# Kernel optimization log

Hardware: AMD Instinct MI355X
Metric: run time of the kernel (lower is better)

Reference implementation:

```python
import jax, jax.numpy as jnp
import numpy as np

NEG_SLOPE = 0.2
F_OUT = 64


def setup_inputs() -> dict:
    key = jax.random.key(0)
    k1, k2, k3 = jax.random.split(key, 3)
    N, F_IN = 8192, 256
    h = jax.random.normal(k1, (N, F_IN), dtype=jnp.float32)
    adj = jnp.ones((N, N), dtype=jnp.bool_)  # unused by the original forward
    # xavier-uniform-ish init scale
    W = jax.random.uniform(k2, (F_IN, F_OUT), dtype=jnp.float32,
                           minval=-1.0, maxval=1.0) * np.sqrt(6.0 / (F_IN + F_OUT))
    a = jax.random.uniform(k3, (2 * F_OUT, 1), dtype=jnp.float32,
                           minval=-1.0, maxval=1.0) * np.sqrt(6.0 / (2 * F_OUT + 1))
    return {"h": h, "adj": adj, "W": W, "a": a}


def reference(h, adj, W, a):
    # Wh: [N, F_OUT]
    Wh = h @ W
    # The torch code materializes an [N*N, F] repeat to compute what is just
    # a broadcast add of two projected score vectors:
    # e[i, j] = leakyrelu(Wh[i] @ a1 + Wh[j] @ a2)
    s1 = Wh @ a[:F_OUT]   # [N, 1]
    s2 = Wh @ a[F_OUT:]   # [N, 1]
    e = s1 + s2.T         # [N, N]
    e = jnp.where(e >= 0, e, NEG_SLOPE * e)  # LeakyReLU(0.2)
    attention = jax.nn.softmax(e, axis=1)    # note: adj is NOT used (matches source)
    return attention @ Wh                    # [N, F_OUT]
```

## Files before the change

### kernel.cpp

```cpp
#include <hip/hip_runtime.h>
#include <math.h>

#define GN 8192
#define GF 64
#define GFIN 256
#define NEG 0.2f
#define NFINE 256
#define FCH 32

#define OFF_WH   0
#define OFF_S1   (GN*GF)
#define OFF_S2   (OFF_S1 + GN)
#define OFF_ZS   (OFF_S2 + GN)
#define OFF_IDX  (OFF_ZS + GN)
#define OFF_FA   (OFF_IDX + GN)
#define OFF_FB   (OFF_FA + NFINE*GF)
#define OFF_FSA  (OFF_FB + NFINE*GF)
#define OFF_FSB  (OFF_FSA + NFINE)
#define OFF_OFA  (OFF_FSB + NFINE)
#define OFF_OFB  (OFF_OFA + NFINE*GF)
#define OFF_OSA  (OFF_OFB + NFINE*GF)
#define OFF_OSB  (OFF_OSA + NFINE)
#define ZERO_CNT (2*NFINE*GF + 2*NFINE)

__global__ __launch_bounds__(512) void k_wh(const float* __restrict__ h,
        const float* __restrict__ W, const float* __restrict__ a,
        float* __restrict__ wsf) {
    float* Wh = wsf + OFF_WH;
    float* s1 = wsf + OFF_S1;
    float* s2 = wsf + OFF_S2;
    __shared__ float WlT[GF*GFIN];
    int t = threadIdx.x, b = blockIdx.x;
    int zm = b*512 + t;
    if (zm < ZERO_CNT) wsf[OFF_FA + zm] = 0.f;
    int lane = t & 63;
    const float4* W4 = (const float4*)W;
    #pragma unroll
    for (int m = 0; m < 8; ++m) {
        int g = t + m*512;
        float4 v = W4[g];
        int k = g >> 4;
        int c0 = (g & 15) * 4;
        WlT[(c0  )*GFIN + (k ^ (((c0  )&7)<<2))] = v.x;
        WlT[(c0+1)*GFIN + (k ^ (((c0+1)&7)<<2))] = v.y;
        WlT[(c0+2)*GFIN + (k ^ (((c0+2)&7)<<2))] = v.z;
        WlT[(c0+3)*GFIN + (k ^ (((c0+3)&7)<<2))] = v.w;
    }
    __syncthreads();
    int wid = __builtin_amdgcn_readfirstlane(t >> 6);
    int row0 = b*32 + wid*4;
    const float* hrow = h + (size_t)row0 * GFIN;
    float acc[4] = {0.f,0.f,0.f,0.f};
    const float4* WlT4 = (const float4*)WlT;
    int cbase = lane * (GFIN/4);
    int sw = lane & 7;
    #pragma unroll 8
    for (int k4 = 0; k4 < GFIN/4; ++k4) {
        float4 wv = WlT4[cbase + (k4 ^ sw)];
        int kk = k4*4;
        #pragma unroll
        for (int q = 0; q < 4; ++q) {
            acc[q] += hrow[q*GFIN + kk  ] * wv.x;
            acc[q] += hrow[q*GFIN + kk+1] * wv.y;
            acc[q] += hrow[q*GFIN + kk+2] * wv.z;
            acc[q] += hrow[q*GFIN + kk+3] * wv.w;
        }
    }
    float a1 = a[lane], a2 = a[GF + lane];
    #pragma unroll
    for (int q = 0; q < 4; ++q) {
        int row = row0 + q;
        Wh[(size_t)row*GF + lane] = acc[q];
        float v1 = acc[q]*a1, v2 = acc[q]*a2;
        #pragma unroll
        for (int o = 32; o > 0; o >>= 1) { v1 += __shfl_xor(v1, o); v2 += __shfl_xor(v2, o); }
        if (lane == 0) { s1[row] = v1; s2[row] = v2; }
    }
}

__global__ __launch_bounds__(512) void k_rank(const float* __restrict__ Whg,
        float* __restrict__ wsf) {
    __shared__ float zl[GN];
    __shared__ int rl[32];
    __shared__ float redm[8];
    const float* s2 = wsf + OFF_S2;
    float* zs = wsf + OFF_ZS;
    int* idx = (int*)(wsf + OFF_IDX);
    float* fineA = wsf + OFF_FA;
    float* fineB = wsf + OFF_FB;
    float* fSA = wsf + OFF_FSA;
    float* fSB = wsf + OFF_FSB;
    int t = threadIdx.x, b = blockIdx.x;
    int lane = t & 63, wid = t >> 6;
    const float4* s4 = (const float4*)s2;
    float4* z4 = (float4*)zl;
    float mx = -1e30f;
    for (int m = t; m < GN/4; m += 512) {
        float4 v = s4[m]; z4[m] = v;
        mx = fmaxf(fmaxf(mx, v.x), fmaxf(fmaxf(v.y, v.z), v.w));
    }
    #pragma unroll
    for (int o = 32; o > 0; o >>= 1) mx = fmaxf(mx, __shfl_xor(mx, o));
    if (lane == 0) redm[wid] = mx;
    __syncthreads();
    float Z = redm[0];
    #pragma unroll
    for (int w2 = 1; w2 < 8; ++w2) Z = fmaxf(Z, redm[w2]);
    int jl = t >> 4, sl = t & 15;
    int j = b*32 + jl;
    float zj = zl[j];
    int cnt = 0;
    #pragma unroll 4
    for (int i = 0; i < GN/64; ++i) {
        int m4 = i*16 + sl;
        float4 v = z4[m4];
        int mb = m4*4;
        cnt += (v.x < zj) || (v.x == zj && mb   < j);
        cnt += (v.y < zj) || (v.y == zj && mb+1 < j);
        cnt += (v.z < zj) || (v.z == zj && mb+2 < j);
        cnt += (v.w < zj) || (v.w == zj && mb+3 < j);
    }
    cnt += __shfl_xor(cnt, 1);
    cnt += __shfl_xor(cnt, 2);
    cnt += __shfl_xor(cnt, 4);
    cnt += __shfl_xor(cnt, 8);
    if (sl == 0) { zs[cnt] = zj; idx[cnt] = j; rl[jl] = cnt; }
    __syncthreads();
    #pragma unroll
    for (int q = 0; q < 4; ++q) {
        int jj = wid*4 + q;
        int jg = b*32 + jj;
        int r = rl[jj];
        float d = zl[jg] - Z;
        float tA = __expf(d);
        float tB = __expf(NEG*d);
        float w = Whg[(size_t)jg*GF + lane];
        int fc = r >> 5;
        atomicAdd(&fineA[fc*GF + lane], tA*w);
        atomicAdd(&fineB[fc*GF + lane], tB*w);
        if (lane == 0) atomicAdd(&fSA[fc], tA);
        if (lane == 1) atomicAdd(&fSB[fc], tB);
    }
}

__global__ __launch_bounds__(256) void k_scan(float* __restrict__ wsf) {
    __shared__ float stg[NFINE];
    __shared__ float wred[4];
    const float* fineA = wsf + OFF_FA;
    const float* fineB = wsf + OFF_FB;
    const float* fSA = wsf + OFF_FSA;
    const float* fSB = wsf + OFF_FSB;
    float* ofA = wsf + OFF_OFA;
    float* ofB = wsf + OFF_OFB;
    float* osA = wsf + OFF_OSA;
    float* osB = wsf + OFF_OSB;
    int c = blockIdx.x;
    int t = threadIdx.x, lane = t & 63, wid = t >> 6;
    float fA = (c < 64) ? fineA[t*GF + c] : fSA[t];
    float fB = (c < 64) ? fineB[t*GF + c] : fSB[t];
    {
        float ws = fB;
        #pragma unroll
        for (int o = 1; o < 64; o <<= 1) { float y = __shfl_up(ws, o); if (lane >= o) ws += y; }
        if (lane == 63) wred[wid] = ws;
        __syncthreads();
        float blkoff = 0.f;
        #pragma unroll
        for (int w2 = 0; w2 < 4; ++w2) { float x = wred[w2]; if (w2 < wid) blkoff += x; }
        float exB = blkoff + ws - fB;
        if (c < 64) ofB[t*GF + c] = exB; else osB[t] = exB;
    }
    __syncthreads();
    stg[t] = fA;
    __syncthreads();
    {
        int rt = NFINE-1-t;
        float vA = stg[rt];
        float ws = vA;
        #pragma unroll
        for (int o = 1; o < 64; o <<= 1) { float y = __shfl_up(ws, o); if (lane >= o) ws += y; }
        __syncthreads();
        if (lane == 63) wred[wid] = ws;
        __syncthreads();
        float blkoff = 0.f;
        #pragma unroll
        for (int w2 = 0; w2 < 4; ++w2) { float x = wred[w2]; if (w2 < wid) blkoff += x; }
        float exA = blkoff + ws - vA;
        if (c < 64) ofA[rt*GF + c] = exA; else osA[rt] = exA;
    }
}

__global__ __launch_bounds__(256) void k_out(const float* __restrict__ wsf,
        float* __restrict__ out) {
    const float* Wh = wsf + OFF_WH;
    const float* s1 = wsf + OFF_S1;
    const float* zs = wsf + OFF_ZS;
    const int* idx = (const int*)(wsf + OFF_IDX);
    const float* ofA = wsf + OFF_OFA;
    const float* ofB = wsf + OFF_OFB;
    const float* osA = wsf + OFF_OSA;
    const float* osB = wsf + OFF_OSB;
    int t = threadIdx.x;
    int wid = t >> 6, lane = t & 63;
    int i = blockIdx.x*4 + wid;
    float s1i = s1[i];
    float Z = zs[GN-1];
    float g = s1i + Z;
    float m = (g >= 0.f) ? g : NEG*g;
    float aA = __expf(g - m);
    float aB = __expf(NEG*g - m);
    float tgt = -s1i;
    int lo = 0, hi = GN;
    #pragma unroll
    for (int it = 0; it < 13; ++it) {
        int mid = (lo + hi) >> 1;
        if (zs[mid] < tgt) lo = mid + 1; else hi = mid;
    }
    int k = lo;
    int fc = __builtin_amdgcn_readfirstlane(min(k >> 5, NFINE-1));
    float va = ofA[fc*GF + lane];
    float vb = ofB[fc*GF + lane];
    float sa = osA[fc], pb = osB[fc];
    #pragma unroll 8
    for (int q = 0; q < FCH; ++q) {
        int r = fc*FCH + q;
        float zr = zs[r];
        int ir = idx[r];
        float w = Wh[(size_t)ir*GF + lane];
        float d = zr - Z;
        if (r >= k) { float tA = __expf(d);     va += tA*w; sa += tA; }
        else        { float tB = __expf(NEG*d); vb += tB*w; pb += tB; }
    }
    out[(size_t)i*GF + lane] = (aA*va + aB*vb) / (aA*sa + aB*pb);
}

extern "C" void kernel_launch(void* const* d_in, const int* in_sizes, int n_in,
                              void* d_out, int out_size, void* d_ws, size_t ws_size,
                              hipStream_t stream) {
    const float* h = (const float*)d_in[0];
    const float* W = (const float*)d_in[2];
    const float* a = (const float*)d_in[3];
    float* wsf = (float*)d_ws;
    float* out = (float*)d_out;

    hipLaunchKernelGGL(k_wh,   dim3(GN/32), dim3(512), 0, stream, h, W, a, wsf);
    hipLaunchKernelGGL(k_rank, dim3(GN/32), dim3(512), 0, stream, wsf + OFF_WH, wsf);
    hipLaunchKernelGGL(k_scan, dim3(65),    dim3(256), 0, stream, wsf);
    hipLaunchKernelGGL(k_out,  dim3(GN/4),  dim3(256), 0, stream, wsf, out);
}
```

Measured before the change: 70.99 us.

## Fuse scan into rank kernel via last-block pattern and simplify Wh matmul

Removes the separate k_scan launch. The last k_rank block to finish, detected with an atomic counter, now computes the prefix and suffix scans over the fine chunk sums. Separately, k_wh drops the swizzled transposed LDS layout for W, uses 256 threads per block, and computes 8 rows per wave with broadcast LDS reads. The aim is to save one launch and its gap and to cheapen the W staging. In exchange the scan runs serially in a single block at the tail of k_rank.

Measured after the change: 181.7 us. +156.0%, slower.

```diff
diff --git a/kernel.cpp b/kernel.cpp
--- a/kernel.cpp
+++ b/kernel.cpp
@@ -7,6 +7,7 @@
 #define NEG 0.2f
 #define NFINE 256
 #define FCH 32
+#define NBLK_RANK 256
 
 #define OFF_WH   0
 #define OFF_S1   (GN*GF)
@@ -17,58 +18,42 @@
 #define OFF_FB   (OFF_FA + NFINE*GF)
 #define OFF_FSA  (OFF_FB + NFINE*GF)
 #define OFF_FSB  (OFF_FSA + NFINE)
-#define OFF_OFA  (OFF_FSB + NFINE)
+#define OFF_CNT  (OFF_FSB + NFINE)
+#define OFF_OFA  (OFF_CNT + 1)
 #define OFF_OFB  (OFF_OFA + NFINE*GF)
 #define OFF_OSA  (OFF_OFB + NFINE*GF)
 #define OFF_OSB  (OFF_OSA + NFINE)
-#define ZERO_CNT (2*NFINE*GF + 2*NFINE)
-
-__global__ __launch_bounds__(512) void k_wh(const float* __restrict__ h,
+#define ZERO_CNT (2*NFINE*GF + 2*NFINE + 1)
+
+__global__ __launch_bounds__(256) void k_wh(const float* __restrict__ h,
         const float* __restrict__ W, const float* __restrict__ a,
         float* __restrict__ wsf) {
     float* Wh = wsf + OFF_WH;
     float* s1 = wsf + OFF_S1;
     float* s2 = wsf + OFF_S2;
-    __shared__ float WlT[GF*GFIN];
+    __shared__ float Wl[GFIN*GF];
     int t = threadIdx.x, b = blockIdx.x;
-    int zm = b*512 + t;
+    int lane = t & 63;
+    int zm = b*256 + t;
     if (zm < ZERO_CNT) wsf[OFF_FA + zm] = 0.f;
-    int lane = t & 63;
     const float4* W4 = (const float4*)W;
-    #pragma unroll
-    for (int m = 0; m < 8; ++m) {
-        int g = t + m*512;
-        float4 v = W4[g];
-        int k = g >> 4;
-        int c0 = (g & 15) * 4;
-        WlT[(c0  )*GFIN + (k ^ (((c0  )&7)<<2))] = v.x;
-        WlT[(c0+1)*GFIN + (k ^ (((c0+1)&7)<<2))] = v.y;
-        WlT[(c0+2)*GFIN + (k ^ (((c0+2)&7)<<2))] = v.z;
-        WlT[(c0+3)*GFIN + (k ^ (((c0+3)&7)<<2))] = v.w;
-    }
+    float4* Wl4 = (float4*)Wl;
+    #pragma unroll
+    for (int m = 0; m < 16; ++m) Wl4[t + m*256] = W4[t + m*256];
     __syncthreads();
     int wid = __builtin_amdgcn_readfirstlane(t >> 6);
-    int row0 = b*32 + wid*4;
+    int row0 = b*32 + wid*8;
     const float* hrow = h + (size_t)row0 * GFIN;
-    float acc[4] = {0.f,0.f,0.f,0.f};
-    const float4* WlT4 = (const float4*)WlT;
-    int cbase = lane * (GFIN/4);
-    int sw = lane & 7;
+    float acc[8] = {0.f,0.f,0.f,0.f,0.f,0.f,0.f,0.f};
     #pragma unroll 8
-    for (int k4 = 0; k4 < GFIN/4; ++k4) {
-        float4 wv = WlT4[cbase + (k4 ^ sw)];
-        int kk = k4*4;
-        #pragma unroll
-        for (int q = 0; q < 4; ++q) {
-            acc[q] += hrow[q*GFIN + kk  ] * wv.x;
-            acc[q] += hrow[q*GFIN + kk+1] * wv.y;
-            acc[q] += hrow[q*GFIN + kk+2] * wv.z;
-            acc[q] += hrow[q*GFIN + kk+3] * wv.w;
-        }
+    for (int k = 0; k < GFIN; ++k) {
+        float wv = Wl[k*GF + lane];
+        #pragma unroll
+        for (int q = 0; q < 8; ++q) acc[q] += hrow[q*GFIN + k] * wv;
     }
     float a1 = a[lane], a2 = a[GF + lane];
     #pragma unroll
-    for (int q = 0; q < 4; ++q) {
+    for (int q = 0; q < 8; ++q) {
         int row = row0 + q;
         Wh[(size_t)row*GF + lane] = acc[q];
         float v1 = acc[q]*a1, v2 = acc[q]*a2;
@@ -83,6 +68,7 @@
     __shared__ float zl[GN];
     __shared__ int rl[32];
     __shared__ float redm[8];
+    __shared__ int lastBlk;
     const float* s2 = wsf + OFF_S2;
     float* zs = wsf + OFF_ZS;
     int* idx = (int*)(wsf + OFF_IDX);
@@ -90,6 +76,11 @@
     float* fineB = wsf + OFF_FB;
     float* fSA = wsf + OFF_FSA;
     float* fSB = wsf + OFF_FSB;
+    int* cnt = (int*)(wsf + OFF_CNT);
+    float* ofA = wsf + OFF_OFA;
+    float* ofB = wsf + OFF_OFB;
+    float* osA = wsf + OFF_OSA;
+    float* osB = wsf + OFF_OSB;
     int t = threadIdx.x, b = blockIdx.x;
     int lane = t & 63, wid = t >> 6;
     const float4* s4 = (const float4*)s2;
@@ -109,22 +100,22 @@
     int jl = t >> 4, sl = t & 15;
     int j = b*32 + jl;
     float zj = zl[j];
-    int cnt = 0;
+    int c0 = 0;
     #pragma unroll 4
     for (int i = 0; i < GN/64; ++i) {
         int m4 = i*16 + sl;
         float4 v = z4[m4];
         int mb = m4*4;
-        cnt += (v.x < zj) || (v.x == zj && mb   < j);
-        cnt += (v.y < zj) || (v.y == zj && mb+1 < j);
-        cnt += (v.z < zj) || (v.z == zj && mb+2 < j);
-        cnt += (v.w < zj) || (v.w == zj && mb+3 < j);
-    }
-    cnt += __shfl_xor(cnt, 1);
-    cnt += __shfl_xor(cnt, 2);
-    cnt += __shfl_xor(cnt, 4);
-    cnt += __shfl_xor(cnt, 8);
-    if (sl == 0) { zs[cnt] = zj; idx[cnt] = j; rl[jl] = cnt; }
+        c0 += (v.x < zj) || (v.x == zj && mb   < j);
+        c0 += (v.y < zj) || (v.y == zj && mb+1 < j);
+        c0 += (v.z < zj) || (v.z == zj && mb+2 < j);
+        c0 += (v.w < zj) || (v.w == zj && mb+3 < j);
+    }
+    c0 += __shfl_xor(c0, 1);
+    c0 += __shfl_xor(c0, 2);
+    c0 += __shfl_xor(c0, 4);
+    c0 += __shfl_xor(c0, 8);
+    if (sl == 0) { zs[c0] = zj; idx[c0] = j; rl[jl] = c0; }
     __syncthreads();
     #pragma unroll
     for (int q = 0; q < 4; ++q) {
@@ -141,52 +132,46 @@
         if (lane == 0) atomicAdd(&fSA[fc], tA);
         if (lane == 1) atomicAdd(&fSB[fc], tB);
     }
-}
-
-__global__ __launch_bounds__(256) void k_scan(float* __restrict__ wsf) {
-    __shared__ float stg[NFINE];
-    __shared__ float wred[4];
-    const float* fineA = wsf + OFF_FA;
-    const float* fineB = wsf + OFF_FB;
-    const float* fSA = wsf + OFF_FSA;
-    const float* fSB = wsf + OFF_FSB;
-    float* ofA = wsf + OFF_OFA;
-    float* ofB = wsf + OFF_OFB;
-    float* osA = wsf + OFF_OSA;
-    float* osB = wsf + OFF_OSB;
-    int c = blockIdx.x;
-    int t = threadIdx.x, lane = t & 63, wid = t >> 6;
-    float fA = (c < 64) ? fineA[t*GF + c] : fSA[t];
-    float fB = (c < 64) ? fineB[t*GF + c] : fSB[t];
-    {
-        float ws = fB;
+    __threadfence();
+    __syncthreads();
+    if (t == 0) lastBlk = (atomicAdd(cnt, 1) == NBLK_RANK-1);
+    __syncthreads();
+    if (!lastBlk) return;
+    for (int c = wid; c <= 64; c += 8) {
+        float v[4];
+        int p0 = lane*4;
+        #pragma unroll
+        for (int e = 0; e < 4; ++e) {
+            int ch = p0 + e;
+            v[e] = atomicAdd((c < 64) ? &fineB[ch*GF + c] : &fSB[ch], 0.f);
+        }
+        float s = v[0]+v[1]+v[2]+v[3];
+        float ws = s;
         #pragma unroll
         for (int o = 1; o < 64; o <<= 1) { float y = __shfl_up(ws, o); if (lane >= o) ws += y; }
-        if (lane == 63) wred[wid] = ws;
-        __syncthreads();
-        float blkoff = 0.f;
-        #pragma unroll
-        for (int w2 = 0; w2 < 4; ++w2) { float x = wred[w2]; if (w2 < wid) blkoff += x; }
-        float exB = blkoff + ws - fB;
-        if (c < 64) ofB[t*GF + c] = exB; else osB[t] = exB;
-    }
-    __syncthreads();
-    stg[t] = fA;
-    __syncthreads();
-    {
-        int rt = NFINE-1-t;
-        float vA = stg[rt];
-        float ws = vA;
+        float run = ws - s;
+        #pragma unroll
+        for (int e = 0; e < 4; ++e) {
+            int ch = p0 + e;
+            if (c < 64) ofB[ch*GF + c] = run; else osB[ch] = run;
+            run += v[e];
+        }
+        #pragma unroll
+        for (int e = 0; e < 4; ++e) {
+            int ch = NFINE-1 - (p0 + e);
+            v[e] = atomicAdd((c < 64) ? &fineA[ch*GF + c] : &fSA[ch], 0.f);
+        }
+        s = v[0]+v[1]+v[2]+v[3];
+        ws = s;
         #pragma unroll
         for (int o = 1; o < 64; o <<= 1) { float y = __shfl_up(ws, o); if (lane >= o) ws += y; }
-        __syncthreads();
-        if (lane == 63) wred[wid] = ws;
-        __syncthreads();
-        float blkoff = 0.f;
-        #pragma unroll
-        for (int w2 = 0; w2 < 4; ++w2) { float x = wred[w2]; if (w2 < wid) blkoff += x; }
-        float exA = blkoff + ws - vA;
-        if (c < 64) ofA[rt*GF + c] = exA; else osA[rt] = exA;
+        run = ws - s;
+        #pragma unroll
+        for (int e = 0; e < 4; ++e) {
+            int ch = NFINE-1 - (p0 + e);
+            if (c < 64) ofA[ch*GF + c] = run; else osA[ch] = run;
+            run += v[e];
+        }
     }
 }
 
@@ -243,8 +228,7 @@
     float* wsf = (float*)d_ws;
     float* out = (float*)d_out;
 
-    hipLaunchKernelGGL(k_wh,   dim3(GN/32), dim3(512), 0, stream, h, W, a, wsf);
+    hipLaunchKernelGGL(k_wh,   dim3(GN/32), dim3(256), 0, stream, h, W, a, wsf);
     hipLaunchKernelGGL(k_rank, dim3(GN/32), dim3(512), 0, stream, wsf + OFF_WH, wsf);
-    hipLaunchKernelGGL(k_scan, dim3(65),    dim3(256), 0, stream, wsf);
     hipLaunchKernelGGL(k_out,  dim3(GN/4),  dim3(256), 0, stream, wsf, out);
 }
```

## Restructure Wh projection: 8 rows per wave, untransposed W in LDS

Applied to the files above, without the earlier changes.

The projection kernel now uses 256-thread blocks with 4 waves, and each wave computes 8 rows instead of 4. W is copied into shared memory as-is, without the swizzled transpose, and each lane reads one W element per k. This removes the transpose-store overhead and doubles per-wave reuse of each W load across rows. The cost is more accumulators, scalar rather than float4 LDS reads, and fewer threads per block.

Result: slower. 72.62 us (+2.3%).

```diff
diff --git a/kernel.cpp b/kernel.cpp
--- a/kernel.cpp
+++ b/kernel.cpp
@@ -23,52 +23,35 @@
 #define OFF_OSB  (OFF_OSA + NFINE)
 #define ZERO_CNT (2*NFINE*GF + 2*NFINE)
 
-__global__ __launch_bounds__(512) void k_wh(const float* __restrict__ h,
+__global__ __launch_bounds__(256) void k_wh(const float* __restrict__ h,
         const float* __restrict__ W, const float* __restrict__ a,
         float* __restrict__ wsf) {
     float* Wh = wsf + OFF_WH;
     float* s1 = wsf + OFF_S1;
     float* s2 = wsf + OFF_S2;
-    __shared__ float WlT[GF*GFIN];
+    __shared__ float Wl[GFIN*GF];
     int t = threadIdx.x, b = blockIdx.x;
-    int zm = b*512 + t;
+    int lane = t & 63;
+    int zm = b*256 + t;
     if (zm < ZERO_CNT) wsf[OFF_FA + zm] = 0.f;
-    int lane = t & 63;
     const float4* W4 = (const float4*)W;
-    #pragma unroll
-    for (int m = 0; m < 8; ++m) {
-        int g = t + m*512;
-        float4 v = W4[g];
-        int k = g >> 4;
-        int c0 = (g & 15) * 4;
-        WlT[(c0  )*GFIN + (k ^ (((c0  )&7)<<2))] = v.x;
-        WlT[(c0+1)*GFIN + (k ^ (((c0+1)&7)<<2))] = v.y;
-        WlT[(c0+2)*GFIN + (k ^ (((c0+2)&7)<<2))] = v.z;
-        WlT[(c0+3)*GFIN + (k ^ (((c0+3)&7)<<2))] = v.w;
-    }
+    float4* Wl4 = (float4*)Wl;
+    #pragma unroll
+    for (int m = 0; m < 16; ++m) Wl4[t + m*256] = W4[t + m*256];
     __syncthreads();
     int wid = __builtin_amdgcn_readfirstlane(t >> 6);
-    int row0 = b*32 + wid*4;
+    int row0 = b*32 + wid*8;
     const float* hrow = h + (size_t)row0 * GFIN;
-    float acc[4] = {0.f,0.f,0.f,0.f};
-    const float4* WlT4 = (const float4*)WlT;
-    int cbase = lane * (GFIN/4);
-    int sw = lane & 7;
+    float acc[8] = {0.f,0.f,0.f,0.f,0.f,0.f,0.f,0.f};
     #pragma unroll 8
-    for (int k4 = 0; k4 < GFIN/4; ++k4) {
-        float4 wv = WlT4[cbase + (k4 ^ sw)];
-        int kk = k4*4;
-        #pragma unroll
-        for (int q = 0; q < 4; ++q) {
-            acc[q] += hrow[q*GFIN + kk  ] * wv.x;
-            acc[q] += hrow[q*GFIN + kk+1] * wv.y;
-            acc[q] += hrow[q*GFIN + kk+2] * wv.z;
-            acc[q] += hrow[q*GFIN + kk+3] * wv.w;
-        }
+    for (int k = 0; k < GFIN; ++k) {
+        float wv = Wl[k*GF + lane];
+        #pragma unroll
+        for (int q = 0; q < 8; ++q) acc[q] += hrow[q*GFIN + k] * wv;
     }
     float a1 = a[lane], a2 = a[GF + lane];
     #pragma unroll
-    for (int q = 0; q < 4; ++q) {
+    for (int q = 0; q < 8; ++q) {
         int row = row0 + q;
         Wh[(size_t)row*GF + lane] = acc[q];
         float v1 = acc[q]*a1, v2 = acc[q]*a2;
@@ -243,7 +226,7 @@
     float* wsf = (float*)d_ws;
     float* out = (float*)d_out;
 
-    hipLaunchKernelGGL(k_wh,   dim3(GN/32), dim3(512), 0, stream, h, W, a, wsf);
+    hipLaunchKernelGGL(k_wh,   dim3(GN/32), dim3(256), 0, stream, h, W, a, wsf);
     hipLaunchKernelGGL(k_rank, dim3(GN/32), dim3(512), 0, stream, wsf + OFF_WH, wsf);
     hipLaunchKernelGGL(k_scan, dim3(65),    dim3(256), 0, stream, wsf);
     hipLaunchKernelGGL(k_out,  dim3(GN/4),  dim3(256), 0, stream, wsf, out);
```
